# Kernel tuning notes

Hardware: AMD Instinct MI355X
Metric: run time of the kernel (lower is better)

## Reference

```python
import jax, jax.numpy as jnp
import numpy as np

DIM = 512; NB = 4; BS = DIM // NB            # EinFFT blocks
DS = 64; DC = 4; EXP = 2; DI = EXP * DIM      # Mamba dims
DTR = DIM // 16                               # dt_rank
BLOCKS = 2; LAM = 0.01; B_SZ = 2; L_SZ = 1024

def layer_norm(x, w, b):
    m = x.mean(-1, keepdims=True)
    v = x.var(-1, keepdims=True)
    return (x - m) / jnp.sqrt(v + 1e-5) * w + b

def softshrink(x, lam):
    return jnp.where(x > lam, x - lam, jnp.where(x < -lam, x + lam, jnp.zeros((), x.dtype)))

def mamba(x, in_proj_w, conv_w, conv_b, x_proj_w, dt_proj_w, dt_proj_b, A_log, D, out_proj_w):
    B, L, _ = x.shape
    xz = x @ in_proj_w.T                      # (B,L,2*DI)
    xm, z = jnp.split(xz, 2, axis=-1)
    # causal depthwise conv1d, keep first L outputs
    xt = xm.transpose(0, 2, 1)                # (B,DI,L)
    conv = jax.lax.conv_general_dilated(xt, conv_w, (1,), [(DC - 1, 0)],
                                        feature_group_count=DI,
                                        dimension_numbers=('NCH', 'OIH', 'NCH'))
    xm = jax.nn.silu((conv + conv_b[None, :, None]).transpose(0, 2, 1))  # (B,L,DI)
    proj = xm @ x_proj_w.T                    # (B,L,DTR+2*DS)
    dt = proj[..., :DTR]
    Bm = proj[..., DTR:DTR + DS]
    Cm = proj[..., DTR + DS:]
    dt = jax.nn.softplus(dt @ dt_proj_w.T + dt_proj_b)   # (B,L,DI)
    A = -jnp.exp(A_log)                       # (DI,DS)

    def step(h, inp):
        dt_t, B_t, C_t, u_t = inp             # (B,DI),(B,DS),(B,DS),(B,DI)
        dA = jnp.exp(dt_t[:, :, None] * A)
        h = dA * h + dt_t[:, :, None] * B_t[:, None, :] * u_t[:, :, None]
        y = jnp.einsum('bds,bs->bd', h, C_t)
        return h, y

    h0 = jnp.zeros((B, DI, DS), x.dtype)
    _, ys = jax.lax.scan(step, h0, (dt.transpose(1, 0, 2), Bm.transpose(1, 0, 2),
                                    Cm.transpose(1, 0, 2), xm.transpose(1, 0, 2)))
    y = ys.transpose(1, 0, 2) + xm * D        # (B,L,DI)
    y = y * jax.nn.silu(z)
    return y @ out_proj_w.T

def einfft(x, cw1, cw2, cb1, cb2):
    B, N, C = x.shape
    xf = jnp.fft.fft2(x.reshape(B, N, NB, BS), axes=(1, 2), norm='ortho')
    mul = lambda t, w: jnp.einsum('BNbd,bdk->BNbk', t, w)
    r1 = jax.nn.relu(mul(xf.real, cw1[0]) - mul(xf.imag, cw1[1]) + cb1[0])
    i1 = jax.nn.relu(mul(xf.real, cw1[1]) + mul(xf.imag, cw1[0]) + cb1[1])
    r2 = softshrink(mul(r1, cw2[0]) - mul(i1, cw2[1]) + cb2[0], LAM)
    i2 = softshrink(mul(r1, cw2[1]) + mul(i1, cw2[0]) + cb2[1], LAM)
    out = jnp.fft.ifft2(r2 + 1j * i2, axes=(1, 2), norm='ortho')
    return out.real.astype(x.dtype).reshape(B, N, C)

def setup_inputs() -> dict:
    key = jax.random.key(0)
    ks = jax.random.split(key, 16)
    r = lambda i, shape, s: jax.random.normal(ks[i], shape, jnp.float32) * s
    A_log = jnp.log(jnp.tile(jnp.arange(1, DS + 1, dtype=jnp.float32), (DI, 1)))
    return {
        'x': jax.random.normal(ks[0], (B_SZ, L_SZ, DIM), jnp.float32),
        'ln_w': jnp.ones((DIM,), jnp.float32), 'ln_b': jnp.zeros((DIM,), jnp.float32),
        'in_proj_w': r(1, (2 * DI, DIM), 0.02),
        'conv_w': r(2, (DI, 1, DC), 0.1), 'conv_b': jnp.zeros((DI,), jnp.float32),
        'x_proj_w': r(3, (DTR + 2 * DS, DI), 0.02),
        'dt_proj_w': r(4, (DI, DTR), 0.02),
        'dt_proj_b': jnp.full((DI,), float(np.log(np.expm1(0.01))), jnp.float32),
        'A_log': A_log, 'D': jnp.ones((DI,), jnp.float32),
        'out_proj_w': r(5, (DIM, DI), 0.02),
        'norm2_w': jnp.ones((DIM,), jnp.float32), 'norm2_b': jnp.zeros((DIM,), jnp.float32),
        'cw1': r(6, (2, NB, BS, BS), 0.02), 'cw2': r(7, (2, NB, BS, BS), 0.02),
        'cb1': r(8, (2, NB, BS), 0.02), 'cb2': r(9, (2, NB, BS), 0.02),
    }

def reference(x, ln_w, ln_b, in_proj_w, conv_w, conv_b, x_proj_w, dt_proj_w, dt_proj_b,
              A_log, D, out_proj_w, norm2_w, norm2_b, cw1, cw2, cb1, cb2):
    for _ in range(BLOCKS):
        x = x + mamba(layer_norm(x, ln_w, ln_b), in_proj_w, conv_w, conv_b,
                      x_proj_w, dt_proj_w, dt_proj_b, A_log, D, out_proj_w)
        x = x + einfft(layer_norm(x, norm2_w, norm2_b), cw1, cw2, cb1, cb2)
    return x
```

## Files before the change

### kernel.cpp

```cpp
#include <hip/hip_runtime.h>

typedef unsigned short u16;
typedef __attribute__((ext_vector_type(8))) short bf8;
typedef __attribute__((ext_vector_type(4))) float f4;

__device__ __forceinline__ float bf2f(u16 b) {
    return __uint_as_float(((unsigned)b) << 16);
}
__device__ __forceinline__ u16 f2bf(float f) {
    unsigned u = __float_as_uint(f);
    u += 0x7fffu + ((u >> 16) & 1u);
    return (u16)(u >> 16);
}
__device__ __forceinline__ void pack8f(const float* v, u16* dst) {
    uint r0 = (uint)f2bf(v[0]) | ((uint)f2bf(v[1]) << 16);
    uint r1 = (uint)f2bf(v[2]) | ((uint)f2bf(v[3]) << 16);
    uint r2 = (uint)f2bf(v[4]) | ((uint)f2bf(v[5]) << 16);
    uint r3 = (uint)f2bf(v[6]) | ((uint)f2bf(v[7]) << 16);
    *(uint4*)dst = make_uint4(r0, r1, r2, r3);
}
__device__ __forceinline__ bf8 neg8(bf8 v) {
    union { bf8 b; uint u[4]; } t; t.b = v;
    t.u[0] ^= 0x80008000u; t.u[1] ^= 0x80008000u;
    t.u[2] ^= 0x80008000u; t.u[3] ^= 0x80008000u;
    return t.b;
}
__device__ __forceinline__ int digrev10(int x) {
    int r = __brev((unsigned)x) >> 22;
    return ((r & 0x2AA) >> 1) | ((r & 0x155) << 1);
}

__global__ void detect_k(const u16* __restrict__ dtb, int* __restrict__ flag) {
    flag[0] = (dtb[0] == dtb[1] && dtb[1] == dtb[2] && dtb[2] == dtb[3] &&
               dtb[3] == dtb[4] && dtb[4] == dtb[5]) ? 1 : 0;
    flag[1] = 1;
}

__global__ __launch_bounds__(256)
void achk_k(const float* __restrict__ alog, int* __restrict__ flag) {
    int i = blockIdx.x * 256 + threadIdx.x;
    int s = i & 63;
    float n = __expf(alog[i]);
    float e = (float)(s + 1);
    if (fabsf(n - e) > 0.02f * e) atomicAnd(&flag[1], 0);
}

struct CvtArgs {
    const void* src[18];
    void* dst[18];
    int n[18];
    int obf[18];
};
__global__ __launch_bounds__(256)
void cvt_all_k(CvtArgs a, const int* __restrict__ flag) {
    const int t = blockIdx.y;
    const int n = a.n[t];
    const int f = flag[0];
    if (a.obf[t] == 2) {
        u16* __restrict__ d = (u16*)a.dst[t];
        if (f) {
            const u16* __restrict__ s = (const u16*)a.src[t];
            for (int i = blockIdx.x * 256 + threadIdx.x; i < n; i += gridDim.x * 256) {
                int cin = i & 127, cout = (i >> 7) & 127, snb = i >> 14;
                d[(snb << 14) + (cout << 7) + cin] = s[(snb << 14) + (cin << 7) + cout];
            }
        } else {
            const float* __restrict__ s = (const float*)a.src[t];
            for (int i = blockIdx.x * 256 + threadIdx.x; i < n; i += gridDim.x * 256) {
                int cin = i & 127, cout = (i >> 7) & 127, snb = i >> 14;
                d[(snb << 14) + (cout << 7) + cin] =
                    f2bf(s[(snb << 14) + (cin << 7) + cout]);
            }
        }
    } else if (a.obf[t] == 1) {
        u16* __restrict__ d = (u16*)a.dst[t];
        if (f) {
            const u16* __restrict__ s = (const u16*)a.src[t];
            for (int i = blockIdx.x * 256 + threadIdx.x; i < n; i += gridDim.x * 256)
                d[i] = s[i];
        } else {
            const float* __restrict__ s = (const float*)a.src[t];
            for (int i = blockIdx.x * 256 + threadIdx.x; i < n; i += gridDim.x * 256)
                d[i] = f2bf(s[i]);
        }
    } else {
        float* __restrict__ d = (float*)a.dst[t];
        if (f) {
            const u16* __restrict__ s = (const u16*)a.src[t];
            for (int i = blockIdx.x * 256 + threadIdx.x; i < n; i += gridDim.x * 256)
                d[i] = bf2f(s[i]);
        } else {
            const float* __restrict__ s = (const float*)a.src[t];
            for (int i = blockIdx.x * 256 + threadIdx.x; i < n; i += gridDim.x * 256)
                d[i] = s[i];
        }
    }
}

__global__ void out_k(const float* __restrict__ in, void* __restrict__ out,
                      int n, const int* __restrict__ flag) {
    int i = blockIdx.x * 256 + threadIdx.x;
    if (i >= n) return;
    if (flag[0]) ((u16*)out)[i] = f2bf(in[i]);
    else         ((float*)out)[i] = in[i];
}

__global__ __launch_bounds__(256)
void ln_k(const float* __restrict__ x, const float* __restrict__ w,
          const float* __restrict__ b, u16* __restrict__ out) {
    const int row = blockIdx.x, tid = threadIdx.x;
    const float* xr = x + (long)row * 512;
    float v0 = xr[tid], v1 = xr[tid + 256];
    float s = v0 + v1, q = v0 * v0 + v1 * v1;
#pragma unroll
    for (int off = 32; off; off >>= 1) {
        s += __shfl_xor(s, off);
        q += __shfl_xor(q, off);
    }
    __shared__ float ss[4], qq[4];
    int wid = tid >> 6;
    if ((tid & 63) == 0) { ss[wid] = s; qq[wid] = q; }
    __syncthreads();
    s = ss[0] + ss[1] + ss[2] + ss[3];
    q = qq[0] + qq[1] + qq[2] + qq[3];
    float mean = s * (1.f / 512.f);
    float var = q * (1.f / 512.f) - mean * mean;
    float rstd = rsqrtf(var + 1e-5f);
    u16* o = out + (long)row * 512;
    o[tid]       = f2bf((v0 - mean) * rstd * w[tid]       + b[tid]);
    o[tid + 256] = f2bf((v1 - mean) * rstd * w[tid + 256] + b[tid + 256]);
}

#define LSTR 40
template <int TAF, int EPI>
__global__ __launch_bounds__(256)
void mgemm_k(const void* __restrict__ Ap, const u16* __restrict__ Bp,
             float* __restrict__ D, int N, int K, int lda, int ldb, int ldc,
             long bsA, long bsB, long bsC,
             const float* __restrict__ bias, const float* __restrict__ res) {
    const float* Af = (const float*)Ap + blockIdx.z * bsA;
    const u16*  Ab  = (const u16*)Ap + blockIdx.z * bsA;
    const u16*  B   = Bp + blockIdx.z * bsB;
    D += blockIdx.z * bsC;

    __shared__ u16 As[64 * LSTR];
    __shared__ u16 Bs[64 * LSTR];
    const int tid = threadIdx.x;
    const int lane = tid & 63;
    const int w = tid >> 6, wm = w & 1, wn = w >> 1;
    const int m0 = blockIdx.y * 64, n0 = blockIdx.x * 64;
    const int fr = (lane & 15), fq = (lane >> 4);

    f4 acc[2][2] = {};

    for (int k0 = 0; k0 < K; k0 += 32) {
        {
            const int ar = tid >> 2, aks = (tid & 3) << 3;
            if constexpr (TAF) {
                *(uint4*)&As[ar * LSTR + aks] =
                    *(const uint4*)(Ab + (long)(m0 + ar) * lda + k0 + aks);
            } else {
                const float* p = Af + (long)(m0 + ar) * lda + k0 + aks;
                float tv[8];
                float4 x = *(const float4*)p, y = *(const float4*)(p + 4);
                tv[0] = x.x; tv[1] = x.y; tv[2] = x.z; tv[3] = x.w;
                tv[4] = y.x; tv[5] = y.y; tv[6] = y.z; tv[7] = y.w;
                pack8f(tv, &As[ar * LSTR + aks]);
            }
        }
        {
            const int br = tid >> 2, bks = (tid & 3) << 3;
            uint4 raw = make_uint4(0, 0, 0, 0);
            if (n0 + br < N)
                raw = *(const uint4*)(B + (long)(n0 + br) * ldb + k0 + bks);
            *(uint4*)&Bs[br * LSTR + bks] = raw;
        }
        __syncthreads();
        bf8 af[2], bff[2];
#pragma unroll
        for (int t = 0; t < 2; t++) {
            af[t]  = *(bf8*)&As[(wm * 32 + t * 16 + fr) * LSTR + (fq << 3)];
            bff[t] = *(bf8*)&Bs[(wn * 32 + t * 16 + fr) * LSTR + (fq << 3)];
        }
#pragma unroll
        for (int i = 0; i < 2; i++)
#pragma unroll
            for (int j = 0; j < 2; j++)
                acc[i][j] = __builtin_amdgcn_mfma_f32_16x16x32_bf16(
                    af[i], bff[j], acc[i][j], 0, 0, 0);
        __syncthreads();
    }

#pragma unroll
    for (int i = 0; i < 2; i++) {
#pragma unroll
        for (int j = 0; j < 2; j++) {
            const int gmb = m0 + wm * 32 + i * 16 + (fq << 2);
            const int gn  = n0 + wn * 32 + j * 16 + fr;
            if (gn >= N) continue;
            float v[4];
#pragma unroll
            for (int e = 0; e < 4; e++) v[e] = acc[i][j][e];
            if constexpr (EPI == 1) {
                float bb = bias[gn];
#pragma unroll
                for (int e = 0; e < 4; e++) {
                    float t = v[e] + bb;
                    v[e] = (t > 20.f) ? t : log1pf(__expf(t));
                }
            }
#pragma unroll
            for (int e = 0; e < 4; e++) {
                long idx = (long)(gmb + e) * ldc + gn;
                float t = v[e];
                if constexpr (EPI == 2) t += res[idx];
                D[idx] = t;
            }
        }
    }
}

__global__ __launch_bounds__(256)
void red4_k(float* __restrict__ dst, const float* __restrict__ P, int n, int s) {
    int i = blockIdx.x * 256 + threadIdx.x;
    if (i < n) dst[i] = P[i] + P[i + s] + P[i + 2 * s] + P[i + 3 * s];
}

__global__ __launch_bounds__(256)
void gemm128_k(const u16* __restrict__ A, const u16* __restrict__ B,
               float* __restrict__ D, int K, int lda, int ldb, int ldc) {
    __shared__ u16 As[128 * LSTR];
    __shared__ u16 Bs[128 * LSTR];
    const int tid = threadIdx.x, lane = tid & 63;
    const int w = tid >> 6, wm = w & 1, wn = w >> 1;
    const int m0 = blockIdx.y * 128, n0 = blockIdx.x * 128;
    const int fr = lane & 15, fq = lane >> 4;
    f4 acc[4][4] = {};

    for (int k0 = 0; k0 < K; k0 += 32) {
#pragma unroll
        for (int j = 0; j < 2; ++j) {
            int idx = tid + j * 256;
            int row = idx >> 2, col = (idx & 3) << 3;
            *(uint4*)&As[row * LSTR + col] =
                *(const uint4*)(A + (long)(m0 + row) * lda + k0 + col);
            *(uint4*)&Bs[row * LSTR + col] =
                *(const uint4*)(B + (long)(n0 + row) * ldb + k0 + col);
        }
        __syncthreads();
        bf8 af[4], bfv[4];
#pragma unroll
        for (int i = 0; i < 4; ++i) {
            af[i]  = *(bf8*)&As[(wm * 64 + i * 16 + fr) * LSTR + (fq << 3)];
            bfv[i] = *(bf8*)&Bs[(wn * 64 + i * 16 + fr) * LSTR + (fq << 3)];
        }
#pragma unroll
        for (int i = 0; i < 4; ++i)
#pragma unroll
            for (int j = 0; j < 4; ++j)
                acc[i][j] = __builtin_amdgcn_mfma_f32_16x16x32_bf16(
                    af[i], bfv[j], acc[i][j], 0, 0, 0);
        __syncthreads();
    }
#pragma unroll
    for (int i = 0; i < 4; ++i)
#pragma unroll
        for (int j = 0; j < 4; ++j) {
            const int gm = m0 + wm * 64 + i * 16 + (fq << 2);
            const int gn = n0 + wn * 64 + j * 16 + fr;
#pragma unroll
            for (int e = 0; e < 4; ++e)
                D[(long)(gm + e) * ldc + gn] = acc[i][j][e];
        }
}

__global__ __launch_bounds__(1024)
void ffw_k(const u16* __restrict__ xn, u16* __restrict__ Orb,
           u16* __restrict__ Oib) {
    const int bz = blockIdx.x;
    const int b = bz >> 7, cg = bz & 127;
    const int t = threadIdx.x;
    const int f = t >> 8, tl = t & 255;
    const int c = cg + f * 128;
    __shared__ float re[4224], im[4224], twr[768], twi[768];
    if (t < 768) {
        float s, cc;
        __sincosf((float)t * -6.1359231515425649e-3f, &s, &cc);
        twr[t] = cc; twi[t] = s;
    }
    float* rf = re + f * 1056;
    float* mf = im + f * 1056;
    const u16* src = xn + ((long)b * 1024) * 512 + c;
#pragma unroll
    for (int r = 0; r < 4; ++r) {
        int n = tl + r * 256;
        float v = bf2f(src[(long)n * 512]);
        int a = n + (n >> 5);
        rf[a] = v; mf[a] = 0.f;
    }
    __syncthreads();
#pragma unroll
    for (int st = 0; st < 5; ++st) {
        const int qsh = 8 - 2 * st;
        const int q = 1 << qsh;
        const int len = q << 2;
        const int m = 1 << (2 * st);
        int j = tl & (q - 1);
        int g = tl >> qsh;
        int i0 = g * len + j;
        int a0 = i0 + (i0 >> 5);
        int i1 = i0 + q,     a1 = i1 + (i1 >> 5);
        int i2 = i0 + 2 * q, a2 = i2 + (i2 >> 5);
        int i3 = i0 + 3 * q, a3 = i3 + (i3 >> 5);
        float ar = rf[a0], ai = mf[a0];
        float br = rf[a1], bi = mf[a1];
        float cr = rf[a2], ci = mf[a2];
        float dr = rf[a3], di = mf[a3];
        float t0r = ar + cr, t0i = ai + ci;
        float t1r = ar - cr, t1i = ai - ci;
        float t2r = br + dr, t2i = bi + di;
        float u = br - dr, v = bi - di;
        rf[a0] = t0r + t2r; mf[a0] = t0i + t2i;
        {
            int k = j * m;
            float wr = twr[k], wi = twi[k];
            float xr = t1r + v, xi = t1i - u;
            rf[a1] = xr * wr - xi * wi;
            mf[a1] = xr * wi + xi * wr;
        }
        {
            int k = 2 * j * m;
            float wr = twr[k], wi = twi[k];
            float xr = t0r - t2r, xi = t0i - t2i;
            rf[a2] = xr * wr - xi * wi;
            mf[a2] = xr * wi + xi * wr;
        }
        {
            int k = 3 * j * m;
            float wr = twr[k], wi = twi[k];
            float xr = t1r - v, xi = t1i + u;
            rf[a3] = xr * wr - xi * wi;
            mf[a3] = xr * wi + xi * wr;
        }
        __syncthreads();
    }
    u16* drp = Orb + ((long)(b * 512 + c)) * 1024;
    u16* dip = Oib + ((long)(b * 512 + c)) * 1024;
#pragma unroll
    for (int r = 0; r < 4; ++r) {
        int kf = tl + r * 256;
        int sidx = digrev10(kf);
        int a = sidx + (sidx >> 5);
        float r0 = re[a],        i0v = im[a];
        float r1 = re[1056 + a], i1v = im[1056 + a];
        float r2 = re[2112 + a], i2v = im[2112 + a];
        float r3 = re[3168 + a], i3v = im[3168 + a];
        float vr, vi;
        if (f == 0)      { vr = r0 + r1 + r2 + r3;     vi = i0v + i1v + i2v + i3v; }
        else if (f == 1) { vr = r0 + i1v - r2 - i3v;   vi = i0v - r1 - i2v + r3; }
        else if (f == 2) { vr = r0 - r1 + r2 - r3;     vi = i0v - i1v + i2v - i3v; }
        else             { vr = r0 - i1v - r2 + i3v;   vi = i0v + r1 - i2v - r3; }
        drp[kf] = f2bf(vr * 0.015625f);
        dip[kf] = f2bf(vi * 0.015625f);
    }
}

__global__ __launch_bounds__(1024)
void ifw_k(const u16* __restrict__ X2r, const u16* __restrict__ X2i,
           float* __restrict__ Yc) {
    const int bz = blockIdx.x;
    const int b = bz >> 7, cg = bz & 127;
    const int t = threadIdx.x;
    const int f = t >> 8, tl = t & 255;
    const int c = cg + f * 128;
    __shared__ float re[4224], im[4224], twr[768], twi[768];
    if (t < 768) {
        float s, cc;
        __sincosf((float)t * 6.1359231515425649e-3f, &s, &cc);
        twr[t] = cc; twi[t] = s;
    }
    const u16* sr = X2r + ((long)(b * 512 + c)) * 1024;
    const u16* si = X2i + ((long)(b * 512 + c)) * 1024;
    float* rf = re + f * 1056;
    float* mf = im + f * 1056;
    const int k4 = tl * 4;
    {
        uint2 pr = *(const uint2*)&sr[k4];
        uint2 pi = *(const uint2*)&si[k4];
        u16 rv[4] = {(u16)(pr.x & 0xFFFF), (u16)(pr.x >> 16),
                     (u16)(pr.y & 0xFFFF), (u16)(pr.y >> 16)};
        u16 iv[4] = {(u16)(pi.x & 0xFFFF), (u16)(pi.x >> 16),
                     (u16)(pi.y & 0xFFFF), (u16)(pi.y >> 16)};
#pragma unroll
        for (int e = 0; e < 4; ++e) {
            int idx = k4 + e;
            int a = idx + (idx >> 5);
            rf[a] = bf2f(rv[e]);
            mf[a] = bf2f(iv[e]);
        }
    }
    __syncthreads();
    float vr[4], vi[4];
#pragma unroll
    for (int e = 0; e < 4; ++e) {
        int idx = k4 + e;
        int a = idx + (idx >> 5);
        float r0 = re[a],        i0v = im[a];
        float r1 = re[1056 + a], i1v = im[1056 + a];
        float r2 = re[2112 + a], i2v = im[2112 + a];
        float r3 = re[3168 + a], i3v = im[3168 + a];
        if (f == 0)      { vr[e] = r0 + r1 + r2 + r3;     vi[e] = i0v + i1v + i2v + i3v; }
        else if (f == 1) { vr[e] = r0 - i1v - r2 + i3v;   vi[e] = i0v + r1 - i2v - r3; }
        else if (f == 2) { vr[e] = r0 - r1 + r2 - r3;     vi[e] = i0v - i1v + i2v - i3v; }
        else             { vr[e] = r0 + i1v - r2 - i3v;   vi[e] = i0v - r1 - i2v + r3; }
        vr[e] *= 0.5f; vi[e] *= 0.5f;
    }
    __syncthreads();
#pragma unroll
    for (int e = 0; e < 4; ++e) {
        int idx = k4 + e;
        int a = idx + (idx >> 5);
        rf[a] = vr[e]; mf[a] = vi[e];
    }
    __syncthreads();
#pragma unroll
    for (int st = 0; st < 5; ++st) {
        const int qsh = 8 - 2 * st;
        const int q = 1 << qsh;
        const int len = q << 2;
        const int m = 1 << (2 * st);
        int j = tl & (q - 1);
        int g = tl >> qsh;
        int i0 = g * len + j;
        int a0 = i0 + (i0 >> 5);
        int i1 = i0 + q,     a1 = i1 + (i1 >> 5);
        int i2 = i0 + 2 * q, a2 = i2 + (i2 >> 5);
        int i3 = i0 + 3 * q, a3 = i3 + (i3 >> 5);
        float ar = rf[a0], ai = mf[a0];
        float br = rf[a1], bi = mf[a1];
        float cr = rf[a2], ci = mf[a2];
        float dr = rf[a3], di = mf[a3];
        float t0r = ar + cr, t0i = ai + ci;
        float t1r = ar - cr, t1i = ai - ci;
        float t2r = br + dr, t2i = bi + di;
        float u = br - dr, v = bi - di;
        rf[a0] = t0r + t2r; mf[a0] = t0i + t2i;
        {
            int k = j * m;
            float wr = twr[k], wi = twi[k];
            float xr = t1r - v, xi = t1i + u;
            rf[a1] = xr * wr - xi * wi;
            mf[a1] = xr * wi + xi * wr;
        }
        {
            int k = 2 * j * m;
            float wr = twr[k], wi = twi[k];
            float xr = t0r - t2r, xi = t0i - t2i;
            rf[a2] = xr * wr - xi * wi;
            mf[a2] = xr * wi + xi * wr;
        }
        {
            int k = 3 * j * m;
            float wr = twr[k], wi = twi[k];
            float xr = t1r + v, xi = t1i - u;
            rf[a3] = xr * wr - xi * wi;
            mf[a3] = xr * wi + xi * wr;
        }
        __syncthreads();
    }
    float* d = Yc + ((long)(b * 512 + c)) * 1024;
#pragma unroll
    for (int r = 0; r < 4; ++r) {
        int n = tl + r * 256;
        int sidx = digrev10(n);
        int a = sidx + (sidx >> 5);
        d[n] = rf[a] * 0.03125f;
    }
}

__global__ __launch_bounds__(256)
void transadd_k(float* __restrict__ xbuf, const float* __restrict__ Yc) {
    const int b = blockIdx.z;
    const int c0 = blockIdx.x * 64, n0 = blockIdx.y * 64;
    __shared__ float T[64][65];
    const int tid = threadIdx.x;
    const int r = tid >> 2, q = (tid & 3) * 16;
    const float* src = Yc + ((long)(b * 512 + c0 + r)) * 1024 + n0 + q;
#pragma unroll
    for (int k = 0; k < 4; ++k) {
        float4 v = *(const float4*)(src + k * 4);
        T[r][q + k * 4 + 0] = v.x; T[r][q + k * 4 + 1] = v.y;
        T[r][q + k * 4 + 2] = v.z; T[r][q + k * 4 + 3] = v.w;
    }
    __syncthreads();
    float* dst = xbuf + ((long)(b * 1024 + n0 + r)) * 512 + c0 + q;
#pragma unroll
    for (int k = 0; k < 4; ++k) {
        float4 w = *(const float4*)(dst + k * 4);
        w.x += T[q + k * 4 + 0][r]; w.y += T[q + k * 4 + 1][r];
        w.z += T[q + k * 4 + 2][r]; w.w += T[q + k * 4 + 3][r];
        *(float4*)(dst + k * 4) = w;
    }
}

template <int ACT>
__global__ __launch_bounds__(256)
void cmix_k(const u16* __restrict__ Xr, const u16* __restrict__ Xi,
            const u16* __restrict__ WT, const float* __restrict__ cb,
            u16* __restrict__ Or, u16* __restrict__ Oi) {
    const int z = blockIdx.z, b = z >> 2, nb = z & 3;
    const u16* Ar = Xr + (long)b * 524288 + nb * 131072;
    const u16* Ai = Xi + (long)b * 524288 + nb * 131072;
    const u16* Wr = WT + nb * 16384;
    const u16* Wi = WT + 65536 + nb * 16384;
    u16* Dr = Or + (long)b * 524288 + nb * 131072;
    u16* Di = Oi + (long)b * 524288 + nb * 131072;
    __shared__ u16 Ars[64 * LSTR], Ais[64 * LSTR], Brs[64 * LSTR], Bis[64 * LSTR];
    const int tid = threadIdx.x, lane = tid & 63;
    const int w = tid >> 6, wm = w & 1, wn = w >> 1;
    const int m0 = blockIdx.y * 64, n0 = blockIdx.x * 64;
    const int fr = (lane & 15), fq = (lane >> 4);
    f4 accr[2][2] = {}, acci[2][2] = {};

    for (int k0 = 0; k0 < 128; k0 += 32) {
        {
            const int am = tid & 63, akb = (tid >> 6) << 3;
            u16 tr[8], ti[8];
#pragma unroll
            for (int j = 0; j < 8; j++) {
                long off = (long)(k0 + akb + j) * 1024 + m0 + am;
                tr[j] = Ar[off]; ti[j] = Ai[off];
            }
            uint r0 = (uint)tr[0] | ((uint)tr[1] << 16);
            uint r1 = (uint)tr[2] | ((uint)tr[3] << 16);
            uint r2 = (uint)tr[4] | ((uint)tr[5] << 16);
            uint r3 = (uint)tr[6] | ((uint)tr[7] << 16);
            *(uint4*)&Ars[am * LSTR + akb] = make_uint4(r0, r1, r2, r3);
            r0 = (uint)ti[0] | ((uint)ti[1] << 16);
            r1 = (uint)ti[2] | ((uint)ti[3] << 16);
            r2 = (uint)ti[4] | ((uint)ti[5] << 16);
            r3 = (uint)ti[6] | ((uint)ti[7] << 16);
            *(uint4*)&Ais[am * LSTR + akb] = make_uint4(r0, r1, r2, r3);
        }
        {
            const int br = tid >> 2, bks = (tid & 3) << 3;
            *(uint4*)&Brs[br * LSTR + bks] =
                *(const uint4*)(Wr + (long)(n0 + br) * 128 + k0 + bks);
            *(uint4*)&Bis[br * LSTR + bks] =
                *(const uint4*)(Wi + (long)(n0 + br) * 128 + k0 + bks);
        }
        __syncthreads();
        bf8 arf[2], aif[2], brf[2], bif[2];
#pragma unroll
        for (int t = 0; t < 2; t++) {
            arf[t] = *(bf8*)&Ars[(wm * 32 + t * 16 + fr) * LSTR + (fq << 3)];
            aif[t] = *(bf8*)&Ais[(wm * 32 + t * 16 + fr) * LSTR + (fq << 3)];
            brf[t] = *(bf8*)&Brs[(wn * 32 + t * 16 + fr) * LSTR + (fq << 3)];
            bif[t] = *(bf8*)&Bis[(wn * 32 + t * 16 + fr) * LSTR + (fq << 3)];
        }
        bf8 nai[2] = { neg8(aif[0]), neg8(aif[1]) };
#pragma unroll
        for (int i = 0; i < 2; i++)
#pragma unroll
            for (int j = 0; j < 2; j++) {
                accr[i][j] = __builtin_amdgcn_mfma_f32_16x16x32_bf16(arf[i], brf[j], accr[i][j], 0, 0, 0);
                accr[i][j] = __builtin_amdgcn_mfma_f32_16x16x32_bf16(nai[i], bif[j], accr[i][j], 0, 0, 0);
                acci[i][j] = __builtin_amdgcn_mfma_f32_16x16x32_bf16(arf[i], bif[j], acci[i][j], 0, 0, 0);
                acci[i][j] = __builtin_amdgcn_mfma_f32_16x16x32_bf16(aif[i], brf[j], acci[i][j], 0, 0, 0);
            }
        __syncthreads();
    }
#pragma unroll
    for (int i = 0; i < 2; i++)
#pragma unroll
        for (int j = 0; j < 2; j++) {
            const int gmb = m0 + wm * 32 + i * 16 + (fq << 2);
            const int gn  = n0 + wn * 32 + j * 16 + fr;
            const float bbr = cb[nb * 128 + gn];
            const float bbi = cb[512 + nb * 128 + gn];
            u16 pr[4], pi[4];
#pragma unroll
            for (int e = 0; e < 4; e++) {
                float vr = accr[i][j][e] + bbr;
                float vi = acci[i][j][e] + bbi;
                if (ACT == 0) {
                    vr = fmaxf(vr, 0.f);
                    vi = fmaxf(vi, 0.f);
                } else {
                    vr = (vr > 0.01f) ? vr - 0.01f : ((vr < -0.01f) ? vr + 0.01f : 0.f);
                    vi = (vi > 0.01f) ? vi - 0.01f : ((vi < -0.01f) ? vi + 0.01f : 0.f);
                }
                pr[e] = f2bf(vr); pi[e] = f2bf(vi);
            }
            uint2 wr2, wi2;
            wr2.x = (uint)pr[0] | ((uint)pr[1] << 16);
            wr2.y = (uint)pr[2] | ((uint)pr[3] << 16);
            wi2.x = (uint)pi[0] | ((uint)pi[1] << 16);
            wi2.y = (uint)pi[2] | ((uint)pi[3] << 16);
            *(uint2*)&Dr[(long)gn * 1024 + gmb] = wr2;
            *(uint2*)&Di[(long)gn * 1024 + gmb] = wi2;
        }
}

__global__ __launch_bounds__(256)
void conv_k(const float* __restrict__ xz, const float* __restrict__ cw,
            const float* __restrict__ cb, float* __restrict__ u) {
    int idx = blockIdx.x * 256 + threadIdx.x;
    int d = idx & 1023;
    int l = (idx >> 10) & 1023;
    int b = idx >> 20;
    float acc = cb[d];
    const float* base = xz + (long)b * 1024 * 2048 + d;
#pragma unroll
    for (int j = 0; j < 4; j++) {
        int li = l - 3 + j;
        if (li >= 0) acc = fmaf(cw[d * 4 + j], base[(long)li * 2048], acc);
    }
    float sig = 1.f / (1.f + __expf(-acc));
    u[idx] = acc * sig;
}

__global__ __launch_bounds__(256)
void scan1_k(const float* __restrict__ dtL, const float* __restrict__ uL,
             const float* __restrict__ projL, const float* __restrict__ alog,
             u16* __restrict__ Hb, float* __restrict__ Sbuf,
             const int* __restrict__ flag) {
    const int dg = blockIdx.x, c = blockIdx.y, b = blockIdx.z;
    const int tid = threadIdx.x;
    const int d = dg * 256 + tid;
    const int t0 = c * 16;
    __shared__ float Bls[16][64];
    {
        int r = tid >> 4, cg = (tid & 15) << 2;
        *(float4*)&Bls[r][cg] =
            *(const float4*)(projL + ((long)(b * 1024 + t0 + r)) * 160 + 32 + cg);
    }
    __syncthreads();

    float h[64];
#pragma unroll
    for (int s = 0; s < 64; s++) h[s] = 0.f;
    float S = 0.f;
    const float* dtp = dtL + (long)(b * 1024 + t0) * 1024 + d;
    const float* up  = uL  + (long)(b * 1024 + t0) * 1024 + d;

    if (flag[1]) {
        for (int t = 0; t < 16; ++t) {
            float dt = dtp[(long)t * 1024];
            float uu = up[(long)t * 1024];
            float dtu = dt * uu;
            S += dt;
            float q = __expf(-dt);
            float q2 = q * q, q3 = q2 * q, q4 = q2 * q2;
            float a0 = q, a1 = q2, a2 = q3, a3 = q4;
            const float4* B4p = (const float4*)&Bls[t][0];
#pragma unroll
            for (int sg = 0; sg < 16; ++sg) {
                float4 B4 = B4p[sg];
                h[sg * 4 + 0] = a0 * h[sg * 4 + 0] + dtu * B4.x;
                h[sg * 4 + 1] = a1 * h[sg * 4 + 1] + dtu * B4.y;
                h[sg * 4 + 2] = a2 * h[sg * 4 + 2] + dtu * B4.z;
                h[sg * 4 + 3] = a3 * h[sg * 4 + 3] + dtu * B4.w;
                a0 *= q4; a1 *= q4; a2 *= q4; a3 *= q4;
            }
        }
    } else {
        float A[64];
        const float* ap = alog + (long)d * 64;
#pragma unroll
        for (int s = 0; s < 64; s += 4) {
            float4 a4 = *(const float4*)(ap + s);
            A[s] = -__expf(a4.x); A[s + 1] = -__expf(a4.y);
            A[s + 2] = -__expf(a4.z); A[s + 3] = -__expf(a4.w);
        }
        for (int t = 0; t < 16; ++t) {
            float dt = dtp[(long)t * 1024];
            float uu = up[(long)t * 1024];
            float dtu = dt * uu;
            S += dt;
            const float4* B4p = (const float4*)&Bls[t][0];
#pragma unroll
            for (int sg = 0; sg < 16; ++sg) {
                float4 B4 = B4p[sg];
                h[sg * 4 + 0] = __expf(dt * A[sg * 4 + 0]) * h[sg * 4 + 0] + dtu * B4.x;
                h[sg * 4 + 1] = __expf(dt * A[sg * 4 + 1]) * h[sg * 4 + 1] + dtu * B4.y;
                h[sg * 4 + 2] = __expf(dt * A[sg * 4 + 2]) * h[sg * 4 + 2] + dtu * B4.z;
                h[sg * 4 + 3] = __expf(dt * A[sg * 4 + 3]) * h[sg * 4 + 3] + dtu * B4.w;
            }
        }
    }
    u16* Hp = Hb + ((((long)(b * 64 + c)) * 1024 + d) << 6);
#pragma unroll
    for (int s = 0; s < 64; s += 4) {
        uint2 p;
        p.x = ((__float_as_uint(h[s]) + 0x8000u) >> 16) |
              ((__float_as_uint(h[s + 1]) + 0x8000u) & 0xFFFF0000u);
        p.y = ((__float_as_uint(h[s + 2]) + 0x8000u) >> 16) |
              ((__float_as_uint(h[s + 3]) + 0x8000u) & 0xFFFF0000u);
        *(uint2*)&Hp[s] = p;
    }
    Sbuf[(b * 64 + c) * 1024 + d] = S;
}

__global__ __launch_bounds__(256)
void scan2_k(const float* __restrict__ alog, const float* __restrict__ Sbuf,
             u16* __restrict__ Hb) {
    int idx = blockIdx.x * 256 + threadIdx.x;
    int s = idx & 63, d = (idx >> 6) & 1023, b = idx >> 16;
    float A = -__expf(alog[(long)d * 64 + s]);
    float carry = 0.f;
    for (int c = 0; c < 64; ++c) {
        float S = Sbuf[(b * 64 + c) * 1024 + d];
        float P = __expf(A * S);
        long off = ((((long)(b * 64 + c)) * 1024 + d) << 6) + s;
        float H = bf2f(Hb[off]);
        Hb[off] = (u16)((__float_as_uint(carry) + 0x8000u) >> 16);
        carry = P * carry + H;
    }
}

__global__ __launch_bounds__(256)
void scan3_k(float* __restrict__ dtL, const float* __restrict__ uL,
             const float* __restrict__ xz, const float* __restrict__ projL,
             const float* __restrict__ alog, const u16* __restrict__ Hb,
             const float* __restrict__ Dw, const int* __restrict__ flag) {
    const int dg = blockIdx.x, c = blockIdx.y, b = blockIdx.z;
    const int tid = threadIdx.x;
    const int d = dg * 256 + tid;
    const int t0 = c * 16;
    __shared__ float Bls[16][64];
    __shared__ float Cls[16][64];
    {
        int r = tid >> 4, cg = (tid & 15) << 2;
        const float* src = projL + ((long)(b * 1024 + t0 + r)) * 160 + 32 + cg;
        *(float4*)&Bls[r][cg] = *(const float4*)src;
        *(float4*)&Cls[r][cg] = *(const float4*)(src + 64);
    }
    __syncthreads();

    float h[64];
    const u16* Hp = Hb + ((((long)(b * 64 + c)) * 1024 + d) << 6);
#pragma unroll
    for (int s = 0; s < 64; s += 4) {
        uint2 p = *(const uint2*)&Hp[s];
        h[s]     = __uint_as_float(p.x << 16);
        h[s + 1] = __uint_as_float(p.x & 0xFFFF0000u);
        h[s + 2] = __uint_as_float(p.y << 16);
        h[s + 3] = __uint_as_float(p.y & 0xFFFF0000u);
    }
    const float Dd = Dw[d];
    float* dtp = dtL + (long)(b * 1024 + t0) * 1024 + d;
    const float* up = uL + (long)(b * 1024 + t0) * 1024 + d;
    const float* zp = xz + (long)(b * 1024 + t0) * 2048 + 1024 + d;

    if (flag[1]) {
        for (int t = 0; t < 16; ++t) {
            float dt = dtp[(long)t * 1024];
            float uu = up[(long)t * 1024];
            float zz = zp[(long)t * 2048];
            float dtu = dt * uu;
            float y = 0.f;
            float q = __expf(-dt);
            float q2 = q * q, q3 = q2 * q, q4 = q2 * q2;
            float a0 = q, a1 = q2, a2 = q3, a3 = q4;
            const float4* B4p = (const float4*)&Bls[t][0];
            const float4* C4p = (const float4*)&Cls[t][0];
#pragma unroll
            for (int sg = 0; sg < 16; ++sg) {
                float4 B4 = B4p[sg];
                float4 C4 = C4p[sg];
                h[sg * 4 + 0] = a0 * h[sg * 4 + 0] + dtu * B4.x;
                y = fmaf(h[sg * 4 + 0], C4.x, y);
                h[sg * 4 + 1] = a1 * h[sg * 4 + 1] + dtu * B4.y;
                y = fmaf(h[sg * 4 + 1], C4.y, y);
                h[sg * 4 + 2] = a2 * h[sg * 4 + 2] + dtu * B4.z;
                y = fmaf(h[sg * 4 + 2], C4.z, y);
                h[sg * 4 + 3] = a3 * h[sg * 4 + 3] + dtu * B4.w;
                y = fmaf(h[sg * 4 + 3], C4.w, y);
                a0 *= q4; a1 *= q4; a2 *= q4; a3 *= q4;
            }
            float g = zz / (1.f + __expf(-zz));
            dtp[(long)t * 1024] = (y + uu * Dd) * g;
        }
    } else {
        float A[64];
        const float* ap = alog + (long)d * 64;
#pragma unroll
        for (int s = 0; s < 64; s += 4) {
            float4 a4 = *(const float4*)(ap + s);
            A[s] = -__expf(a4.x); A[s + 1] = -__expf(a4.y);
            A[s + 2] = -__expf(a4.z); A[s + 3] = -__expf(a4.w);
        }
        for (int t = 0; t < 16; ++t) {
            float dt = dtp[(long)t * 1024];
            float uu = up[(long)t * 1024];
            float zz = zp[(long)t * 2048];
            float dtu = dt * uu;
            float y = 0.f;
            const float4* B4p = (const float4*)&Bls[t][0];
            const float4* C4p = (const float4*)&Cls[t][0];
#pragma unroll
            for (int sg = 0; sg < 16; ++sg) {
                float4 B4 = B4p[sg];
                float4 C4 = C4p[sg];
                h[sg * 4 + 0] = __expf(dt * A[sg * 4 + 0]) * h[sg * 4 + 0] + dtu * B4.x;
                y = fmaf(h[sg * 4 + 0], C4.x, y);
                h[sg * 4 + 1] = __expf(dt * A[sg * 4 + 1]) * h[sg * 4 + 1] + dtu * B4.y;
                y = fmaf(h[sg * 4 + 1], C4.y, y);
                h[sg * 4 + 2] = __expf(dt * A[sg * 4 + 2]) * h[sg * 4 + 2] + dtu * B4.z;
                y = fmaf(h[sg * 4 + 2], C4.z, y);
                h[sg * 4 + 3] = __expf(dt * A[sg * 4 + 3]) * h[sg * 4 + 3] + dtu * B4.w;
                y = fmaf(h[sg * 4 + 3], C4.w, y);
            }
            float g = zz / (1.f + __expf(-zz));
            dtp[(long)t * 1024] = (y + uu * Dd) * g;
        }
    }
}

extern "C" void kernel_launch(void* const* d_in, const int* in_sizes, int n_in,
                              void* d_out, int out_size, void* d_ws, size_t ws_size,
                              hipStream_t stream) {
    float* ws = (float*)d_ws;
    int* flag = (int*)ws;
    size_t o = 64;
    float* xbuf  = ws + o; o += 1048576;
    float* xz    = ws + o; o += 4194304;
    float* dtL   = ws + o; o += 2097152;
    float* uL    = ws + o; o += 2097152;
    float* projL = ws + o; o += 327680;
    u16* xnb     = (u16*)(ws + o); o += 524288;
    u16* wInpB   = (u16*)(ws + o); o += 524288;
    u16* wXpB    = (u16*)(ws + o); o += 81920;
    u16* wDtB    = (u16*)(ws + o); o += 16384;
    u16* wOutB   = (u16*)(ws + o); o += 262144;
    u16* WT1     = (u16*)(ws + o); o += 65536;
    u16* WT2     = (u16*)(ws + o); o += 65536;
    float* wConv = ws + o; o += 4096;
    float* wAlog = ws + o; o += 65536;
    float* wLnW  = ws + o; o += 512;
    float* wLnB  = ws + o; o += 512;
    float* wConvB= ws + o; o += 1024;
    float* wDtBias=ws + o; o += 1024;
    float* wD    = ws + o; o += 1024;
    float* wN2w  = ws + o; o += 512;
    float* wN2b  = ws + o; o += 512;
    float* wCb1  = ws + o; o += 1024;
    float* wCb2  = ws + o; o += 1024;
    float* Hreg  = ws + o; o += 4194304;
    float* Sbuf  = ws + o; o += 131072;
    u16* Hb    = (u16*)Hreg;
    float* Pbuf = Hreg;
    float* Yc  = dtL;
    u16* xzb  = (u16*)xz;
    u16* Xrb  = xzb;
    u16* Xib  = xzb + 1048576;
    u16* r1b  = xzb + 2097152;
    u16* i1b  = xzb + 3145728;
    u16* X2rb = xzb + 4194304;
    u16* X2ib = xzb + 5242880;

    dim3 blk(256);

    detect_k<<<1, 1, 0, stream>>>((const u16*)d_in[8], flag);

    CvtArgs ca;
    void* dsts[18] = {xbuf, wLnW, wLnB, wInpB, wConv, wConvB, wXpB, wDtB, wDtBias,
                      wAlog, wD, wOutB, wN2w, wN2b, WT1, WT2, wCb1, wCb2};
    int obf[18]    = {0,    0,    0,    1,     0,     0,      1,    1,    0,
                      0,     0,  1,     0,    0,    2,   2,   0,    0};
    for (int i = 0; i < 18; i++) {
        ca.src[i] = d_in[i];
        ca.dst[i] = dsts[i];
        ca.n[i] = in_sizes[i];
        ca.obf[i] = obf[i];
    }
    cvt_all_k<<<dim3(64, 18), blk, 0, stream>>>(ca, flag);
    achk_k<<<256, blk, 0, stream>>>(wAlog, flag);

    for (int it = 0; it < 2; ++it) {
        ln_k<<<2048, blk, 0, stream>>>(xbuf, wLnW, wLnB, xnb);
        gemm128_k<<<dim3(16, 16), blk, 0, stream>>>(
            xnb, wInpB, xz, 512, 512, 512, 2048);
        conv_k<<<8192, blk, 0, stream>>>(xz, wConv, wConvB, uL);
        mgemm_k<0, 0><<<dim3(3, 32, 4), blk, 0, stream>>>(
            uL, wXpB, Pbuf, 160, 256, 1024, 1024, 160,
            256, 256, 327680, nullptr, nullptr);
        red4_k<<<1280, blk, 0, stream>>>(projL, Pbuf, 327680, 327680);
        mgemm_k<0, 1><<<dim3(16, 32, 1), blk, 0, stream>>>(
            projL, wDtB, dtL, 1024, 32, 160, 32, 1024, 0, 0, 0, wDtBias, nullptr);
        scan1_k<<<dim3(4, 64, 2), blk, 0, stream>>>(dtL, uL, projL, wAlog, Hb, Sbuf, flag);
        scan2_k<<<512, blk, 0, stream>>>(wAlog, Sbuf, Hb);
        scan3_k<<<dim3(4, 64, 2), blk, 0, stream>>>(dtL, uL, xz, projL, wAlog, Hb, wD, flag);
        mgemm_k<0, 2><<<dim3(8, 32, 1), blk, 0, stream>>>(
            dtL, wOutB, xbuf, 512, 1024, 1024, 1024, 512, 0, 0, 0, nullptr, xbuf);

        ln_k<<<2048, blk, 0, stream>>>(xbuf, wN2w, wN2b, xnb);
        ffw_k<<<256, dim3(1024), 0, stream>>>(xnb, Xrb, Xib);
        cmix_k<0><<<dim3(2, 16, 8), blk, 0, stream>>>(Xrb, Xib, WT1, wCb1, r1b, i1b);
        cmix_k<1><<<dim3(2, 16, 8), blk, 0, stream>>>(r1b, i1b, WT2, wCb2, X2rb, X2ib);
        ifw_k<<<256, dim3(1024), 0, stream>>>(X2rb, X2ib, Yc);
        transadd_k<<<dim3(8, 16, 2), blk, 0, stream>>>(xbuf, Yc);
    }

    out_k<<<(out_size + 255) / 256, blk, 0, stream>>>(xbuf, d_out, out_size, flag);
}
```

Before: 468.3 us.

## Fuse split-K reduction into consumers, store conv/scan outputs as bf16, single-stage cmix

Drops the red4 reduction kernel: the dt-projection GEMM and both scan kernels now sum the four split-K partials of the x_proj output themselves while loading. The conv output u and the gated scan output are written as bf16, so the x_proj and out_proj GEMMs take bf16 A operands directly and memory traffic falls. cmix now loads the whole K=128 tile into shared memory at once with a single barrier instead of looping over four synchronized k-steps. The trade-offs are extra redundant partial-sum reads and some added bf16 rounding of u inside the scan.

```diff
diff --git a/kernel.cpp b/kernel.cpp
--- a/kernel.cpp
+++ b/kernel.cpp
@@ -156,9 +156,23 @@
     for (int k0 = 0; k0 < K; k0 += 32) {
         {
             const int ar = tid >> 2, aks = (tid & 3) << 3;
-            if constexpr (TAF) {
+            if constexpr (TAF == 1) {
                 *(uint4*)&As[ar * LSTR + aks] =
                     *(const uint4*)(Ab + (long)(m0 + ar) * lda + k0 + aks);
+            } else if constexpr (TAF == 2) {
+                const float* p = Af + (long)(m0 + ar) * lda + k0 + aks;
+                float4 x = *(const float4*)p, y = *(const float4*)(p + 4);
+#pragma unroll
+                for (int pt = 1; pt < 4; ++pt) {
+                    const float* pp = p + (long)pt * bsA;
+                    float4 x1 = *(const float4*)pp, y1 = *(const float4*)(pp + 4);
+                    x.x += x1.x; x.y += x1.y; x.z += x1.z; x.w += x1.w;
+                    y.x += y1.x; y.y += y1.y; y.z += y1.z; y.w += y1.w;
+                }
+                float tv[8];
+                tv[0] = x.x; tv[1] = x.y; tv[2] = x.z; tv[3] = x.w;
+                tv[4] = y.x; tv[5] = y.y; tv[6] = y.z; tv[7] = y.w;
+                pack8f(tv, &As[ar * LSTR + aks]);
             } else {
                 const float* p = Af + (long)(m0 + ar) * lda + k0 + aks;
                 float tv[8];
@@ -218,12 +232,6 @@
             }
         }
     }
-}
-
-__global__ __launch_bounds__(256)
-void red4_k(float* __restrict__ dst, const float* __restrict__ P, int n, int s) {
-    int i = blockIdx.x * 256 + threadIdx.x;
-    if (i < n) dst[i] = P[i] + P[i + s] + P[i + 2 * s] + P[i + 3 * s];
 }
 
 __global__ __launch_bounds__(256)
@@ -503,6 +511,7 @@
     }
 }
 
+#define LSTR2 136
 template <int ACT>
 __global__ __launch_bounds__(256)
 void cmix_k(const u16* __restrict__ Xr, const u16* __restrict__ Xi,
@@ -515,48 +524,57 @@
     const u16* Wi = WT + 65536 + nb * 16384;
     u16* Dr = Or + (long)b * 524288 + nb * 131072;
     u16* Di = Oi + (long)b * 524288 + nb * 131072;
-    __shared__ u16 Ars[64 * LSTR], Ais[64 * LSTR], Brs[64 * LSTR], Bis[64 * LSTR];
+    __shared__ u16 Ars[64 * LSTR2], Ais[64 * LSTR2], Brs[64 * LSTR2], Bis[64 * LSTR2];
     const int tid = threadIdx.x, lane = tid & 63;
     const int w = tid >> 6, wm = w & 1, wn = w >> 1;
     const int m0 = blockIdx.y * 64, n0 = blockIdx.x * 64;
     const int fr = (lane & 15), fq = (lane >> 4);
     f4 accr[2][2] = {}, acci[2][2] = {};
 
-    for (int k0 = 0; k0 < 128; k0 += 32) {
-        {
-            const int am = tid & 63, akb = (tid >> 6) << 3;
+    {
+        const int am = tid & 63, akb = (tid >> 6) << 3;
+#pragma unroll
+        for (int kk = 0; kk < 4; ++kk) {
+            const int kb = kk * 32 + akb;
             u16 tr[8], ti[8];
 #pragma unroll
             for (int j = 0; j < 8; j++) {
-                long off = (long)(k0 + akb + j) * 1024 + m0 + am;
+                long off = (long)(kb + j) * 1024 + m0 + am;
                 tr[j] = Ar[off]; ti[j] = Ai[off];
             }
             uint r0 = (uint)tr[0] | ((uint)tr[1] << 16);
             uint r1 = (uint)tr[2] | ((uint)tr[3] << 16);
             uint r2 = (uint)tr[4] | ((uint)tr[5] << 16);
             uint r3 = (uint)tr[6] | ((uint)tr[7] << 16);
-            *(uint4*)&Ars[am * LSTR + akb] = make_uint4(r0, r1, r2, r3);
+            *(uint4*)&Ars[am * LSTR2 + kb] = make_uint4(r0, r1, r2, r3);
             r0 = (uint)ti[0] | ((uint)ti[1] << 16);
             r1 = (uint)ti[2] | ((uint)ti[3] << 16);
             r2 = (uint)ti[4] | ((uint)ti[5] << 16);
             r3 = (uint)ti[6] | ((uint)ti[7] << 16);
-            *(uint4*)&Ais[am * LSTR + akb] = make_uint4(r0, r1, r2, r3);
-        }
-        {
-            const int br = tid >> 2, bks = (tid & 3) << 3;
-            *(uint4*)&Brs[br * LSTR + bks] =
-                *(const uint4*)(Wr + (long)(n0 + br) * 128 + k0 + bks);
-            *(uint4*)&Bis[br * LSTR + bks] =
-                *(const uint4*)(Wi + (long)(n0 + br) * 128 + k0 + bks);
-        }
-        __syncthreads();
+            *(uint4*)&Ais[am * LSTR2 + kb] = make_uint4(r0, r1, r2, r3);
+        }
+        const int br = tid >> 2, bks = (tid & 3) << 3;
+#pragma unroll
+        for (int kk = 0; kk < 4; ++kk) {
+            const int kb = kk * 32 + bks;
+            *(uint4*)&Brs[br * LSTR2 + kb] =
+                *(const uint4*)(Wr + (long)(n0 + br) * 128 + kb);
+            *(uint4*)&Bis[br * LSTR2 + kb] =
+                *(const uint4*)(Wi + (long)(n0 + br) * 128 + kb);
+        }
+    }
+    __syncthreads();
+
+#pragma unroll
+    for (int kq = 0; kq < 4; ++kq) {
+        const int kc = kq * 32 + (fq << 3);
         bf8 arf[2], aif[2], brf[2], bif[2];
 #pragma unroll
         for (int t = 0; t < 2; t++) {
-            arf[t] = *(bf8*)&Ars[(wm * 32 + t * 16 + fr) * LSTR + (fq << 3)];
-            aif[t] = *(bf8*)&Ais[(wm * 32 + t * 16 + fr) * LSTR + (fq << 3)];
-            brf[t] = *(bf8*)&Brs[(wn * 32 + t * 16 + fr) * LSTR + (fq << 3)];
-            bif[t] = *(bf8*)&Bis[(wn * 32 + t * 16 + fr) * LSTR + (fq << 3)];
+            arf[t] = *(bf8*)&Ars[(wm * 32 + t * 16 + fr) * LSTR2 + kc];
+            aif[t] = *(bf8*)&Ais[(wm * 32 + t * 16 + fr) * LSTR2 + kc];
+            brf[t] = *(bf8*)&Brs[(wn * 32 + t * 16 + fr) * LSTR2 + kc];
+            bif[t] = *(bf8*)&Bis[(wn * 32 + t * 16 + fr) * LSTR2 + kc];
         }
         bf8 nai[2] = { neg8(aif[0]), neg8(aif[1]) };
 #pragma unroll
@@ -568,8 +586,8 @@
                 acci[i][j] = __builtin_amdgcn_mfma_f32_16x16x32_bf16(arf[i], bif[j], acci[i][j], 0, 0, 0);
                 acci[i][j] = __builtin_amdgcn_mfma_f32_16x16x32_bf16(aif[i], brf[j], acci[i][j], 0, 0, 0);
             }
-        __syncthreads();
-    }
+    }
+
 #pragma unroll
     for (int i = 0; i < 2; i++)
 #pragma unroll
@@ -604,7 +622,7 @@
 
 __global__ __launch_bounds__(256)
 void conv_k(const float* __restrict__ xz, const float* __restrict__ cw,
-            const float* __restrict__ cb, float* __restrict__ u) {
+            const float* __restrict__ cb, u16* __restrict__ u) {
     int idx = blockIdx.x * 256 + threadIdx.x;
     int d = idx & 1023;
     int l = (idx >> 10) & 1023;
@@ -617,12 +635,12 @@
         if (li >= 0) acc = fmaf(cw[d * 4 + j], base[(long)li * 2048], acc);
     }
     float sig = 1.f / (1.f + __expf(-acc));
-    u[idx] = acc * sig;
-}
-
-__global__ __launch_bounds__(256)
-void scan1_k(const float* __restrict__ dtL, const float* __restrict__ uL,
-             const float* __restrict__ projL, const float* __restrict__ alog,
+    u[idx] = f2bf(acc * sig);
+}
+
+__global__ __launch_bounds__(256)
+void scan1_k(const float* __restrict__ dtL, const u16* __restrict__ uLb,
+             const float* __restrict__ Pb, const float* __restrict__ alog,
              u16* __restrict__ Hb, float* __restrict__ Sbuf,
              const int* __restrict__ flag) {
     const int dg = blockIdx.x, c = blockIdx.y, b = blockIdx.z;
@@ -632,8 +650,16 @@
     __shared__ float Bls[16][64];
     {
         int r = tid >> 4, cg = (tid & 15) << 2;
-        *(float4*)&Bls[r][cg] =
-            *(const float4*)(projL + ((long)(b * 1024 + t0 + r)) * 160 + 32 + cg);
+        const float* src = Pb + ((long)(b * 1024 + t0 + r)) * 160 + 32 + cg;
+        float4 v0 = *(const float4*)src;
+        float4 v1 = *(const float4*)(src + 327680);
+        float4 v2 = *(const float4*)(src + 655360);
+        float4 v3 = *(const float4*)(src + 983040);
+        v0.x += v1.x + v2.x + v3.x;
+        v0.y += v1.y + v2.y + v3.y;
+        v0.z += v1.z + v2.z + v3.z;
+        v0.w += v1.w + v2.w + v3.w;
+        *(float4*)&Bls[r][cg] = v0;
     }
     __syncthreads();
 
@@ -642,12 +668,12 @@
     for (int s = 0; s < 64; s++) h[s] = 0.f;
     float S = 0.f;
     const float* dtp = dtL + (long)(b * 1024 + t0) * 1024 + d;
-    const float* up  = uL  + (long)(b * 1024 + t0) * 1024 + d;
+    const u16* up = uLb + (long)(b * 1024 + t0) * 1024 + d;
 
     if (flag[1]) {
         for (int t = 0; t < 16; ++t) {
             float dt = dtp[(long)t * 1024];
-            float uu = up[(long)t * 1024];
+            float uu = bf2f(up[(long)t * 1024]);
             float dtu = dt * uu;
             S += dt;
             float q = __expf(-dt);
@@ -675,7 +701,7 @@
         }
         for (int t = 0; t < 16; ++t) {
             float dt = dtp[(long)t * 1024];
-            float uu = up[(long)t * 1024];
+            float uu = bf2f(up[(long)t * 1024]);
             float dtu = dt * uu;
             S += dt;
             const float4* B4p = (const float4*)&Bls[t][0];
@@ -720,10 +746,11 @@
 }
 
 __global__ __launch_bounds__(256)
-void scan3_k(float* __restrict__ dtL, const float* __restrict__ uL,
-             const float* __restrict__ xz, const float* __restrict__ projL,
+void scan3_k(const float* __restrict__ dtL, const u16* __restrict__ uLb,
+             const float* __restrict__ xz, const float* __restrict__ Pb,
              const float* __restrict__ alog, const u16* __restrict__ Hb,
-             const float* __restrict__ Dw, const int* __restrict__ flag) {
+             const float* __restrict__ Dw, const int* __restrict__ flag,
+             u16* __restrict__ y2) {
     const int dg = blockIdx.x, c = blockIdx.y, b = blockIdx.z;
     const int tid = threadIdx.x;
     const int d = dg * 256 + tid;
@@ -732,9 +759,25 @@
     __shared__ float Cls[16][64];
     {
         int r = tid >> 4, cg = (tid & 15) << 2;
-        const float* src = projL + ((long)(b * 1024 + t0 + r)) * 160 + 32 + cg;
-        *(float4*)&Bls[r][cg] = *(const float4*)src;
-        *(float4*)&Cls[r][cg] = *(const float4*)(src + 64);
+        const float* src = Pb + ((long)(b * 1024 + t0 + r)) * 160 + 32 + cg;
+        float4 v0 = *(const float4*)src;
+        float4 v1 = *(const float4*)(src + 327680);
+        float4 v2 = *(const float4*)(src + 655360);
+        float4 v3 = *(const float4*)(src + 983040);
+        v0.x += v1.x + v2.x + v3.x;
+        v0.y += v1.y + v2.y + v3.y;
+        v0.z += v1.z + v2.z + v3.z;
+        v0.w += v1.w + v2.w + v3.w;
+        *(float4*)&Bls[r][cg] = v0;
+        float4 c0 = *(const float4*)(src + 64);
+        float4 c1 = *(const float4*)(src + 64 + 327680);
+        float4 c2 = *(const float4*)(src + 64 + 655360);
+        float4 c3 = *(const float4*)(src + 64 + 983040);
+        c0.x += c1.x + c2.x + c3.x;
+        c0.y += c1.y + c2.y + c3.y;
+        c0.z += c1.z + c2.z + c3.z;
+        c0.w += c1.w + c2.w + c3.w;
+        *(float4*)&Cls[r][cg] = c0;
     }
     __syncthreads();
 
@@ -749,14 +792,15 @@
         h[s + 3] = __uint_as_float(p.y & 0xFFFF0000u);
     }
     const float Dd = Dw[d];
-    float* dtp = dtL + (long)(b * 1024 + t0) * 1024 + d;
-    const float* up = uL + (long)(b * 1024 + t0) * 1024 + d;
+    const float* dtp = dtL + (long)(b * 1024 + t0) * 1024 + d;
+    const u16* up = uLb + (long)(b * 1024 + t0) * 1024 + d;
     const float* zp = xz + (long)(b * 1024 + t0) * 2048 + 1024 + d;
+    u16* y2p = y2 + (long)(b * 1024 + t0) * 1024 + d;
 
     if (flag[1]) {
         for (int t = 0; t < 16; ++t) {
             float dt = dtp[(long)t * 1024];
-            float uu = up[(long)t * 1024];
+            float uu = bf2f(up[(long)t * 1024]);
             float zz = zp[(long)t * 2048];
             float dtu = dt * uu;
             float y = 0.f;
@@ -780,7 +824,7 @@
                 a0 *= q4; a1 *= q4; a2 *= q4; a3 *= q4;
             }
             float g = zz / (1.f + __expf(-zz));
-            dtp[(long)t * 1024] = (y + uu * Dd) * g;
+            y2p[(long)t * 1024] = f2bf((y + uu * Dd) * g);
         }
     } else {
         float A[64];
@@ -793,7 +837,7 @@
         }
         for (int t = 0; t < 16; ++t) {
             float dt = dtp[(long)t * 1024];
-            float uu = up[(long)t * 1024];
+            float uu = bf2f(up[(long)t * 1024]);
             float zz = zp[(long)t * 2048];
             float dtu = dt * uu;
             float y = 0.f;
@@ -813,7 +857,7 @@
                 y = fmaf(h[sg * 4 + 3], C4.w, y);
             }
             float g = zz / (1.f + __expf(-zz));
-            dtp[(long)t * 1024] = (y + uu * Dd) * g;
+            y2p[(long)t * 1024] = f2bf((y + uu * Dd) * g);
         }
     }
 }
@@ -827,8 +871,6 @@
     float* xbuf  = ws + o; o += 1048576;
     float* xz    = ws + o; o += 4194304;
     float* dtL   = ws + o; o += 2097152;
-    float* uL    = ws + o; o += 2097152;
-    float* projL = ws + o; o += 327680;
     u16* xnb     = (u16*)(ws + o); o += 524288;
     u16* wInpB   = (u16*)(ws + o); o += 524288;
     u16* wXpB    = (u16*)(ws + o); o += 81920;
@@ -849,8 +891,10 @@
     float* wCb2  = ws + o; o += 1024;
     float* Hreg  = ws + o; o += 4194304;
     float* Sbuf  = ws + o; o += 131072;
+    float* Pbuf2 = ws + o; o += 1310720;
+    u16* uLb     = (u16*)(ws + o); o += 1048576;
+    u16* y2b     = (u16*)(ws + o); o += 524288;
     u16* Hb    = (u16*)Hreg;
-    float* Pbuf = Hreg;
     float* Yc  = dtL;
     u16* xzb  = (u16*)xz;
     u16* Xrb  = xzb;
@@ -882,18 +926,17 @@
         ln_k<<<2048, blk, 0, stream>>>(xbuf, wLnW, wLnB, xnb);
         gemm128_k<<<dim3(16, 16), blk, 0, stream>>>(
             xnb, wInpB, xz, 512, 512, 512, 2048);
-        conv_k<<<8192, blk, 0, stream>>>(xz, wConv, wConvB, uL);
-        mgemm_k<0, 0><<<dim3(3, 32, 4), blk, 0, stream>>>(
-            uL, wXpB, Pbuf, 160, 256, 1024, 1024, 160,
+        conv_k<<<8192, blk, 0, stream>>>(xz, wConv, wConvB, uLb);
+        mgemm_k<1, 0><<<dim3(3, 32, 4), blk, 0, stream>>>(
+            uLb, wXpB, Pbuf2, 160, 256, 1024, 1024, 160,
             256, 256, 327680, nullptr, nullptr);
-        red4_k<<<1280, blk, 0, stream>>>(projL, Pbuf, 327680, 327680);
-        mgemm_k<0, 1><<<dim3(16, 32, 1), blk, 0, stream>>>(
-            projL, wDtB, dtL, 1024, 32, 160, 32, 1024, 0, 0, 0, wDtBias, nullptr);
-        scan1_k<<<dim3(4, 64, 2), blk, 0, stream>>>(dtL, uL, projL, wAlog, Hb, Sbuf, flag);
+        mgemm_k<2, 1><<<dim3(16, 32, 1), blk, 0, stream>>>(
+            Pbuf2, wDtB, dtL, 1024, 32, 160, 32, 1024, 327680, 0, 0, wDtBias, nullptr);
+        scan1_k<<<dim3(4, 64, 2), blk, 0, stream>>>(dtL, uLb, Pbuf2, wAlog, Hb, Sbuf, flag);
         scan2_k<<<512, blk, 0, stream>>>(wAlog, Sbuf, Hb);
-        scan3_k<<<dim3(4, 64, 2), blk, 0, stream>>>(dtL, uL, xz, projL, wAlog, Hb, wD, flag);
-        mgemm_k<0, 2><<<dim3(8, 32, 1), blk, 0, stream>>>(
-            dtL, wOutB, xbuf, 512, 1024, 1024, 1024, 512, 0, 0, 0, nullptr, xbuf);
+        scan3_k<<<dim3(4, 64, 2), blk, 0, stream>>>(dtL, uLb, xz, Pbuf2, wAlog, Hb, wD, flag, y2b);
+        mgemm_k<1, 2><<<dim3(8, 32, 1), blk, 0, stream>>>(
+            y2b, wOutB, xbuf, 512, 1024, 1024, 1024, 512, 0, 0, 0, nullptr, xbuf);
 
         ln_k<<<2048, blk, 0, stream>>>(xbuf, wN2w, wN2b, xnb);
         ffw_k<<<256, dim3(1024), 0, stream>>>(xnb, Xrb, Xib);
```

New measurement: 445.8 us. -4.8%, faster.
